# Kernel optimization log

Measured on AMD Instinct MI355X. Metric: run time of the kernel, lower is better.

## Reference

```python
import jax, jax.numpy as jnp
import numpy as np

BETA = 0.25


def setup_inputs() -> dict:
    key = jax.random.key(0)
    k1, k2 = jax.random.split(key)
    inputs = jax.random.normal(k1, (32, 4096, 64), dtype=jnp.float32)
    # VarianceScaling(uniform) ~ small-magnitude init; plain normal scaled works for a numeric reference
    codebook = jax.random.normal(k2, (1024, 64), dtype=jnp.float32) * (1.0 / np.sqrt(64.0))
    return {"inputs": inputs, "codebook": codebook}


def reference(inputs, codebook):
    D = codebook.shape[-1]
    flat = jnp.reshape(inputs, (-1, D))                      # [N, D]
    flat_sqr = jnp.sum(flat ** 2, axis=-1, keepdims=True)    # [N, 1]
    code_sqr = jnp.sum(codebook ** 2, axis=-1)[None, :]      # [1, K]
    # full pairwise squared distances [N, K]
    distances = flat_sqr - 2.0 * (flat @ codebook.T) + code_sqr
    encoding_indices = jnp.reshape(jnp.argmin(distances, axis=-1), inputs.shape[:-1])
    quantize = codebook[encoding_indices]                    # gather -> [..., D]
    encoding_loss = jnp.mean((jax.lax.stop_gradient(inputs) - quantize) ** 2)
    commit_loss = jnp.mean((inputs - jax.lax.stop_gradient(quantize)) ** 2)
    loss = encoding_loss + BETA * commit_loss
    # straight-through estimator
    z_q = inputs + jax.lax.stop_gradient(quantize - inputs)
    return loss, z_q, encoding_indices
```

## Files before the change

kernel.cpp:

```cpp
#include <hip/hip_runtime.h>

#define N_ROWS 131072
#define D 64
#define K_CODES 1024

typedef _Float16 f16x8 __attribute__((ext_vector_type(8)));
typedef float    f32x4 __attribute__((ext_vector_type(4)));

#define MFMA16(a, b, c) __builtin_amdgcn_mfma_f32_16x16x32_f16((a), (b), (c), 0, 0, 0)

__global__ __launch_bounds__(256)
void prep_kernel(const float* __restrict__ CB, _Float16* __restrict__ CBf,
                 float* __restrict__ csqr, float* __restrict__ loss) {
    const int b = blockIdx.x, t = threadIdx.x;
    if (b < 64) {
        const int unit = b * 256 + t;
        const int tile = unit >> 8;
        const int f    = (unit >> 6) & 3;
        const int lane = unit & 63;
        const int quad = lane >> 4, lrow = lane & 15;
        const int code = tile * 16 + lrow;
        const int k0   = (f & 1) * 32 + quad * 8;
        const float* src = CB + (size_t)code * D + k0;
        float4 v0 = *(const float4*)(src);
        float4 v1 = *(const float4*)(src + 4);
        float xs[8] = {v0.x, v0.y, v0.z, v0.w, v1.x, v1.y, v1.z, v1.w};
        f16x8 o;
#pragma unroll
        for (int j = 0; j < 8; ++j) {
            float sv = -2.0f * xs[j];
            _Float16 h = (_Float16)sv;
            o[j] = (f < 2) ? h : (_Float16)(sv - (float)h);
        }
        *(f16x8*)(CBf + (size_t)unit * 8) = o;
    } else {
        if (t == 0) *loss = 0.0f;
        for (int k = t; k < K_CODES; k += 256) {
            const float4* p = (const float4*)(CB + (size_t)k * D);
            float s = 0.0f;
#pragma unroll
            for (int i = 0; i < 16; ++i) {
                float4 v = p[i];
                s += v.x * v.x + v.y * v.y + v.z * v.z + v.w * v.w;
            }
            csqr[k] = s;
        }
    }
}

__device__ __forceinline__ void gload_lds16(const void* g, void* l) {
    __builtin_amdgcn_global_load_lds(
        (const __attribute__((address_space(1))) void*)g,
        (__attribute__((address_space(3))) void*)l,
        16, 0, 0);
}

__global__ __launch_bounds__(512, 4)
void argmin_kernel(const float* __restrict__ X,
                   const _Float16* __restrict__ CBf,
                   const float* __restrict__ csqr,
                   const float* __restrict__ CB,
                   float* __restrict__ out) {
    __shared__ _Float16 Bbuf[16][2048];
    __shared__ float LsC[K_CODES];
    __shared__ int   ivfin[256];
    __shared__ float lsum[8];

    const int t    = threadIdx.x;
    const int wave = t >> 6;
    const int lane = t & 63;
    const int quad = lane >> 4;
    const int lrow = lane & 15;
    const int R0   = blockIdx.x * 256;
    const int Rw   = R0 + wave * 32;

#define STAGE(p_)                                                             \
    do {                                                                      \
        _Pragma("unroll")                                                     \
        for (int i_ = 0; i_ < 8; ++i_) {                                      \
            const int u_ = i_ * 512 + t;                                      \
            const f16x8* gp_ =                                                \
                (const f16x8*)CBf + (size_t)((p_) * 4096 + u_);               \
            gload_lds16((const void*)gp_,                                     \
                        (void*)((char*)&Bbuf[0][0] + (size_t)u_ * 16));       \
        }                                                                     \
    } while (0)

    STAGE(0);

    if (t < 256) ((float4*)LsC)[t] = ((const float4*)csqr)[t];

    f16x8 Ah[2][2], Al[2][2];
    float xsq = 0.0f;
#pragma unroll
    for (int mt = 0; mt < 2; ++mt) {
        const float* xr = X + (size_t)(Rw + mt * 16 + lrow) * D;
#pragma unroll
        for (int ks = 0; ks < 2; ++ks) {
            const int k0 = ks * 32 + quad * 8;
            float4 v0 = *(const float4*)(xr + k0);
            float4 v1 = *(const float4*)(xr + k0 + 4);
            float xs[8] = {v0.x, v0.y, v0.z, v0.w, v1.x, v1.y, v1.z, v1.w};
            f16x8 h, l;
#pragma unroll
            for (int j = 0; j < 8; ++j) {
                xsq += xs[j] * xs[j];
                _Float16 hh = (_Float16)xs[j];
                h[j] = hh;
                l[j] = (_Float16)(xs[j] - (float)hh);
            }
            Ah[mt][ks] = h;
            Al[mt][ks] = l;
        }
    }

    float bestd[2][4];
    int   besti[2][4];
#pragma unroll
    for (int mt = 0; mt < 2; ++mt)
#pragma unroll
        for (int r = 0; r < 4; ++r) { bestd[mt][r] = 3.0e38f; besti[mt][r] = 0; }

    __syncthreads();

    for (int p = 0; p < 4; ++p) {
        if (p) {
            __syncthreads();
            STAGE(p);
            asm volatile("s_waitcnt vmcnt(0)" ::: "memory");
            __syncthreads();
        }
#pragma unroll 4
        for (int i = 0; i < 16; ++i) {
            const f16x8* Bt = (const f16x8*)&Bbuf[i][0] + lane;
            f16x8 b0 = Bt[0], b1 = Bt[64], b2 = Bt[128], b3 = Bt[192];
            const int   c  = (p * 16 + i) * 16 + lrow;
            const float cs = LsC[c];
#pragma unroll
            for (int mt = 0; mt < 2; ++mt) {
                f32x4 acc = {cs, cs, cs, cs};
                acc = MFMA16(Ah[mt][0], b0, acc);
                acc = MFMA16(Ah[mt][1], b1, acc);
                acc = MFMA16(Al[mt][0], b0, acc);
                acc = MFMA16(Al[mt][1], b1, acc);
                acc = MFMA16(Ah[mt][0], b2, acc);
                acc = MFMA16(Ah[mt][1], b3, acc);
#pragma unroll
                for (int r = 0; r < 4; ++r) {
                    bool lt = acc[r] < bestd[mt][r];
                    bestd[mt][r] = lt ? acc[r] : bestd[mt][r];
                    besti[mt][r] = lt ? c : besti[mt][r];
                }
            }
        }
    }

    float dvsum = 0.0f;
#pragma unroll
    for (int mt = 0; mt < 2; ++mt) {
#pragma unroll
        for (int r = 0; r < 4; ++r) {
            float dv = bestd[mt][r];
            int   iv = besti[mt][r];
#pragma unroll
            for (int m = 1; m < 16; m <<= 1) {
                float od = __shfl_xor(dv, m, 64);
                int   oi = __shfl_xor(iv, m, 64);
                if (od < dv || (od == dv && oi < iv)) { dv = od; iv = oi; }
            }
            if (lrow == 0) {
                const int rl = wave * 32 + mt * 16 + quad * 4 + r;
                ivfin[rl] = iv;
                out[1 + (size_t)N_ROWS * D + R0 + rl] = (float)iv;
                dvsum += dv;
            }
        }
    }

    {
        float s = xsq + dvsum;
#pragma unroll
        for (int m = 1; m < 64; m <<= 1) s += __shfl_xor(s, m, 64);
        if (lane == 0) lsum[wave] = s;
    }
    __syncthreads();

    const float scale = 1.25f / (float)((size_t)N_ROWS * D);
    if (t == 0) {
        float L = 0.0f;
#pragma unroll
        for (int w = 0; w < 8; ++w) L += lsum[w];
        atomicAdd(out, L * scale);
    }

    float* p = out + 1 + (size_t)R0 * D;
#pragma unroll
    for (int i = 0; i < 8; ++i) {
        int q = i * 512 + t;
        int j = 4 * q + 3;
        if (q < 4095) {
            float v[4];
#pragma unroll
            for (int e = 0; e < 4; ++e) {
                int jj = j + e;
                v[e] = CB[(size_t)ivfin[jj >> 6] * D + (jj & 63)];
            }
            *(float4*)(p + j) = make_float4(v[0], v[1], v[2], v[3]);
        } else if (q == 4095) {
            p[16383] = CB[(size_t)ivfin[255] * D + 63];
        }
    }
    if (t == 0) {
        const float* c0 = CB + (size_t)ivfin[0] * D;
        p[0] = c0[0];
        p[1] = c0[1];
        p[2] = c0[2];
    }
}

extern "C" void kernel_launch(void* const* d_in, const int* in_sizes, int n_in,
                              void* d_out, int out_size, void* d_ws,
                              size_t ws_size, hipStream_t stream) {
    const float* X  = (const float*)d_in[0];
    const float* CB = (const float*)d_in[1];

    float*    csqr = (float*)d_ws;
    _Float16* CBf  = (_Float16*)((char*)d_ws + 4096);

    hipLaunchKernelGGL(prep_kernel, dim3(65), dim3(256), 0, stream,
                       CB, CBf, csqr, (float*)d_out);
    hipLaunchKernelGGL(argmin_kernel, dim3(N_ROWS / 256), dim3(512), 0, stream,
                       X, CBf, csqr, CB, (float*)d_out);
}
```

Baseline: 142.8 us.

## Fuse codebook fp16 conversion and norms into argmin kernel staging

Drops the separate prep kernel. Each argmin block now reads the fp32 codebook directly, splits it into fp16 hi/lo parts and computes the code norms while staging into LDS. The loss accumulator is zeroed with a memset instead. This removes one kernel launch and the workspace round trip. In exchange, all 512 blocks redo the conversion and norm work, the async global-to-LDS loads become synchronous register loads, and the occupancy hint drops from 4 to 2.

```diff
diff --git a/kernel.cpp b/kernel.cpp
--- a/kernel.cpp
+++ b/kernel.cpp
@@ -9,56 +9,8 @@
 
 #define MFMA16(a, b, c) __builtin_amdgcn_mfma_f32_16x16x32_f16((a), (b), (c), 0, 0, 0)
 
-__global__ __launch_bounds__(256)
-void prep_kernel(const float* __restrict__ CB, _Float16* __restrict__ CBf,
-                 float* __restrict__ csqr, float* __restrict__ loss) {
-    const int b = blockIdx.x, t = threadIdx.x;
-    if (b < 64) {
-        const int unit = b * 256 + t;
-        const int tile = unit >> 8;
-        const int f    = (unit >> 6) & 3;
-        const int lane = unit & 63;
-        const int quad = lane >> 4, lrow = lane & 15;
-        const int code = tile * 16 + lrow;
-        const int k0   = (f & 1) * 32 + quad * 8;
-        const float* src = CB + (size_t)code * D + k0;
-        float4 v0 = *(const float4*)(src);
-        float4 v1 = *(const float4*)(src + 4);
-        float xs[8] = {v0.x, v0.y, v0.z, v0.w, v1.x, v1.y, v1.z, v1.w};
-        f16x8 o;
-#pragma unroll
-        for (int j = 0; j < 8; ++j) {
-            float sv = -2.0f * xs[j];
-            _Float16 h = (_Float16)sv;
-            o[j] = (f < 2) ? h : (_Float16)(sv - (float)h);
-        }
-        *(f16x8*)(CBf + (size_t)unit * 8) = o;
-    } else {
-        if (t == 0) *loss = 0.0f;
-        for (int k = t; k < K_CODES; k += 256) {
-            const float4* p = (const float4*)(CB + (size_t)k * D);
-            float s = 0.0f;
-#pragma unroll
-            for (int i = 0; i < 16; ++i) {
-                float4 v = p[i];
-                s += v.x * v.x + v.y * v.y + v.z * v.z + v.w * v.w;
-            }
-            csqr[k] = s;
-        }
-    }
-}
-
-__device__ __forceinline__ void gload_lds16(const void* g, void* l) {
-    __builtin_amdgcn_global_load_lds(
-        (const __attribute__((address_space(1))) void*)g,
-        (__attribute__((address_space(3))) void*)l,
-        16, 0, 0);
-}
-
-__global__ __launch_bounds__(512, 4)
+__global__ __launch_bounds__(512, 2)
 void argmin_kernel(const float* __restrict__ X,
-                   const _Float16* __restrict__ CBf,
-                   const float* __restrict__ csqr,
                    const float* __restrict__ CB,
                    float* __restrict__ out) {
     __shared__ _Float16 Bbuf[16][2048];
@@ -74,21 +26,47 @@
     const int R0   = blockIdx.x * 256;
     const int Rw   = R0 + wave * 32;
 
-#define STAGE(p_)                                                             \
+#define STAGE_CONV(p_)                                                        \
     do {                                                                      \
         _Pragma("unroll")                                                     \
-        for (int i_ = 0; i_ < 8; ++i_) {                                      \
-            const int u_ = i_ * 512 + t;                                      \
-            const f16x8* gp_ =                                                \
-                (const f16x8*)CBf + (size_t)((p_) * 4096 + u_);               \
-            gload_lds16((const void*)gp_,                                     \
-                        (void*)((char*)&Bbuf[0][0] + (size_t)u_ * 16));       \
+        for (int j_ = 0; j_ < 4; ++j_) {                                      \
+            const int pi_ = (t >> 6) + 8 * j_;                                \
+            const int i_  = pi_ >> 1;                                         \
+            const int fb_ = pi_ & 1;                                          \
+            const int code_ = (p_) * 256 + i_ * 16 + lrow;                    \
+            const int k0_   = fb_ * 32 + quad * 8;                            \
+            const float* src_ = CB + (size_t)code_ * D + k0_;                 \
+            float4 v0_ = *(const float4*)(src_);                              \
+            float4 v1_ = *(const float4*)(src_ + 4);                          \
+            float xs_[8] = {v0_.x, v0_.y, v0_.z, v0_.w,                       \
+                            v1_.x, v1_.y, v1_.z, v1_.w};                      \
+            f16x8 h_, l_;                                                     \
+            _Pragma("unroll")                                                 \
+            for (int e_ = 0; e_ < 8; ++e_) {                                  \
+                float sv_ = -2.0f * xs_[e_];                                  \
+                _Float16 hh_ = (_Float16)sv_;                                 \
+                h_[e_] = hh_;                                                 \
+                l_[e_] = (_Float16)(sv_ - (float)hh_);                        \
+            }                                                                 \
+            _Float16* b_ = &Bbuf[0][0];                                       \
+            *(f16x8*)(b_ + ((size_t)((i_ * 4 + fb_) * 64 + lane)) * 8) = h_;  \
+            *(f16x8*)(b_ + ((size_t)((i_ * 4 + fb_ + 2) * 64 + lane)) * 8)    \
+                = l_;                                                         \
+        }                                                                     \
+        if (t < 256) {                                                        \
+            const int c_ = (p_) * 256 + t;                                    \
+            const float4* q_ = (const float4*)(CB + (size_t)c_ * D);          \
+            float s_ = 0.0f;                                                  \
+            _Pragma("unroll")                                                 \
+            for (int ii_ = 0; ii_ < 16; ++ii_) {                              \
+                float4 v_ = q_[ii_];                                          \
+                s_ += v_.x * v_.x + v_.y * v_.y + v_.z * v_.z + v_.w * v_.w;  \
+            }                                                                 \
+            LsC[c_] = s_;                                                     \
         }                                                                     \
     } while (0)
 
-    STAGE(0);
-
-    if (t < 256) ((float4*)LsC)[t] = ((const float4*)csqr)[t];
+    STAGE_CONV(0);
 
     f16x8 Ah[2][2], Al[2][2];
     float xsq = 0.0f;
@@ -126,8 +104,7 @@
     for (int p = 0; p < 4; ++p) {
         if (p) {
             __syncthreads();
-            STAGE(p);
-            asm volatile("s_waitcnt vmcnt(0)" ::: "memory");
+            STAGE_CONV(p);
             __syncthreads();
         }
 #pragma unroll 4
@@ -224,11 +201,8 @@
     const float* X  = (const float*)d_in[0];
     const float* CB = (const float*)d_in[1];
 
-    float*    csqr = (float*)d_ws;
-    _Float16* CBf  = (_Float16*)((char*)d_ws + 4096);
-
-    hipLaunchKernelGGL(prep_kernel, dim3(65), dim3(256), 0, stream,
-                       CB, CBf, csqr, (float*)d_out);
+    hipMemsetAsync(d_out, 0, sizeof(float), stream);
+
     hipLaunchKernelGGL(argmin_kernel, dim3(N_ROWS / 256), dim3(512), 0, stream,
-                       X, CBf, csqr, CB, (float*)d_out);
+                       X, CB, (float*)d_out);
 }
```

Result: slower. 162.9 us (+14.1%).
